# Performance work log

Hardware: AMD Instinct MI355X
Metric: run time of the kernel (lower is better)

Reference implementation:

```python
import jax, jax.numpy as jnp
import numpy as np

N, E, D = 40000, 640000, 128  # n_nodes, n_edges, hidden_dim
EPS = 1e-5  # equinox RMSNorm default eps


def setup_inputs() -> dict:
    key = jax.random.key(0)
    k1, k2, k3, k4 = jax.random.split(key, 4)
    x = jax.random.normal(k1, (N, D), dtype=jnp.float32)
    e = jax.random.randint(k2, (E, 2), 0, N)  # [E,2] int, col0=src, col1=dst
    W = jax.random.normal(k3, (D, D), dtype=jnp.float32) / np.sqrt(D).astype(np.float32)
    b = jax.random.normal(k4, (D,), dtype=jnp.float32) * 0.01
    g = jnp.ones((D,), dtype=jnp.float32)   # RMSNorm weight
    rb = jnp.zeros((D,), dtype=jnp.float32)  # RMSNorm bias
    return {"x": x, "e": e, "W": W, "b": b, "g": g, "rb": rb}


def reference(x, e, W, b, g, rb):
    src, dst = e[:, 0], e[:, 1]
    # gather source nodes, per-edge linear + relu  -> [E, D]
    m = jax.nn.relu(x[src] @ W.T + b)
    n = x.shape[0]
    # degree (any column of segment_sum(ones_like(m)) is the scalar degree)
    deg = jax.ops.segment_sum(jnp.ones((e.shape[0],), x.dtype), dst, num_segments=n)
    # max-aggregate messages to destination nodes  -> [N, D]
    agg = jax.ops.segment_max(m, dst, num_segments=n)
    agg = jnp.where(deg[:, None] == 0, jnp.zeros((), x.dtype), agg)
    # residual + RMSNorm
    h = x + agg
    inv = jax.lax.rsqrt(jnp.mean(h * h, axis=-1, keepdims=True) + EPS)
    return h * inv * g + rb
```

## Files before the change

### kernel.cpp

```cpp
#include <hip/hip_runtime.h>
#include <hip/hip_bf16.h>

#define D 128
#define EPS 1e-5f

typedef __bf16 bf16x8 __attribute__((ext_vector_type(8)));
typedef __bf16 bf16x4 __attribute__((ext_vector_type(4)));
typedef float  f32x4  __attribute__((ext_vector_type(4)));

__global__ __launch_bounds__(256) void prep_kernel(
    const float* __restrict__ W, __bf16* __restrict__ Wb,
    int* __restrict__ counts, int n)
{
    const int tid = blockIdx.x * 256 + threadIdx.x;

    if (tid < 4096) {
        float4 v = ((const float4*)W)[tid];
        bf16x4 h;
        h[0] = (__bf16)v.x; h[1] = (__bf16)v.y;
        h[2] = (__bf16)v.z; h[3] = (__bf16)v.w;
        ((bf16x4*)Wb)[tid] = h;
    }
    for (int i = tid; i < n; i += 4096)
        counts[i] = 0;
}

__global__ __launch_bounds__(256) void gemm_kernel(
    const float* __restrict__ x, const __bf16* __restrict__ Wb,
    const float* __restrict__ b, __bf16* __restrict__ y,
    const int* __restrict__ e, int* __restrict__ counts,
    int n, int E)
{
    __shared__ __attribute__((aligned(16))) float xs[64][132];

    const int tid  = threadIdx.x;
    const int row0b = blockIdx.x * 64;

    for (int i = tid; i < 2048; i += 256) {
        int r = i >> 5, q = i & 31;
        int gr = row0b + r;
        float4 v = make_float4(0.f, 0.f, 0.f, 0.f);
        if (gr < n) v = ((const float4*)x)[(size_t)gr * 32 + q];
        *(float4*)&xs[r][q * 4] = v;
    }

    {
        const int base   = blockIdx.x * 256 + tid;
        const int stride = gridDim.x * 256;
        for (int i = base; i < E; i += stride)
            atomicAdd(&counts[e[2 * i + 1]], 1);
    }
    __syncthreads();

    const int w  = tid >> 6;
    const int l  = tid & 63;
    const int lr = l & 15;
    const int lk = l >> 4;
    const int row0 = row0b + w * 16;

    bf16x8 a[4];
#pragma unroll
    for (int ks = 0; ks < 4; ks++) {
        const float* p = &xs[w * 16 + lr][ks * 32 + lk * 8];
        float4 v0 = *(const float4*)p;
        float4 v1 = *(const float4*)(p + 4);
        bf16x8 t;
        t[0] = (__bf16)v0.x; t[1] = (__bf16)v0.y;
        t[2] = (__bf16)v0.z; t[3] = (__bf16)v0.w;
        t[4] = (__bf16)v1.x; t[5] = (__bf16)v1.y;
        t[6] = (__bf16)v1.z; t[7] = (__bf16)v1.w;
        a[ks] = t;
    }

#pragma unroll
    for (int ct = 0; ct < 8; ct++) {
        f32x4 acc = {0.f, 0.f, 0.f, 0.f};
#pragma unroll
        for (int ks = 0; ks < 4; ks++) {
            bf16x8 bf = *(const bf16x8*)(Wb + (ct * 16 + lr) * D + ks * 32 + lk * 8);
            acc = __builtin_amdgcn_mfma_f32_16x16x32_bf16(a[ks], bf, acc, 0, 0, 0);
        }
        const int col  = ct * 16 + lr;
        const float bias = b[col];
        const int gr0  = row0 + lk * 4;
#pragma unroll
        for (int reg = 0; reg < 4; reg++) {
            int gr = gr0 + reg;
            if (gr < n)
                y[(size_t)gr * D + col] = (__bf16)fmaxf(acc[reg] + bias, 0.f);
        }
    }
}

__global__ __launch_bounds__(256) void scan_partial_kernel(
    const int* __restrict__ counts, int* __restrict__ row_start,
    int* __restrict__ partials, int n)
{
    __shared__ int s[256];
    const int tid = threadIdx.x;
    const int i = blockIdx.x * 256 + tid;
    int v = (i < n) ? counts[i] : 0;
    s[tid] = v;
    __syncthreads();
    for (int off = 1; off < 256; off <<= 1) {
        int add = (tid >= off) ? s[tid - off] : 0;
        __syncthreads();
        s[tid] += add;
        __syncthreads();
    }
    if (i < n) row_start[i] = s[tid] - v;
    if (tid == 255) partials[blockIdx.x] = s[255];
}

__global__ __launch_bounds__(256) void scan_add_kernel(
    int* __restrict__ row_start, const int* __restrict__ partials,
    int* __restrict__ cursor, int n, int nb)
{
    __shared__ int s[256];
    const int tid = threadIdx.x;
    int v = (tid < nb) ? partials[tid] : 0;
    s[tid] = v;
    __syncthreads();
    for (int off = 1; off < 256; off <<= 1) {
        int add = (tid >= off) ? s[tid - off] : 0;
        __syncthreads();
        s[tid] += add;
        __syncthreads();
    }
    int off0 = (blockIdx.x == 0) ? 0 : s[blockIdx.x - 1];

    if (blockIdx.x == 0 && tid == 0)
        row_start[n] = s[255];

    int i = blockIdx.x * 256 + tid;
    if (i < n) {
        int val = row_start[i] + off0;
        row_start[i] = val;
        cursor[i]    = val;
    }
}

__global__ __launch_bounds__(256) void place_kernel(
    const int* __restrict__ e, int* __restrict__ cursor,
    unsigned short* __restrict__ sorted_src, int E)
{
    int i = blockIdx.x * 256 + threadIdx.x;
    if (i < E) {
        int2 ed = ((const int2*)e)[i];
        int pos = atomicAdd(&cursor[ed.y], 1);
        sorted_src[pos] = (unsigned short)ed.x;
    }
}

__global__ __launch_bounds__(256) void seg_max_finalize_kernel(
    const int* __restrict__ row_start, const unsigned short* __restrict__ ssrc,
    const unsigned int* __restrict__ ybu, const float* __restrict__ x,
    const float* __restrict__ g, const float* __restrict__ rb,
    float* __restrict__ out, int n)
{
    int row  = blockIdx.x * 4 + (threadIdx.x >> 6);
    int lane = threadIdx.x & 63;
    if (row >= n) return;

    const int start = row_start[row];
    const int end   = row_start[row + 1];

    float mx = 0.f, my = 0.f;
    int k = start;
    const int end8 = start + ((end - start) & ~7);
    for (; k < end8; k += 8) {
        unsigned int u0, u1, u2, u3, u4, u5, u6, u7;
        {
            int s0 = ssrc[k + 0], s1 = ssrc[k + 1], s2 = ssrc[k + 2], s3 = ssrc[k + 3];
            int s4 = ssrc[k + 4], s5 = ssrc[k + 5], s6 = ssrc[k + 6], s7 = ssrc[k + 7];
            u0 = ybu[(size_t)s0 * 64 + lane];
            u1 = ybu[(size_t)s1 * 64 + lane];
            u2 = ybu[(size_t)s2 * 64 + lane];
            u3 = ybu[(size_t)s3 * 64 + lane];
            u4 = ybu[(size_t)s4 * 64 + lane];
            u5 = ybu[(size_t)s5 * 64 + lane];
            u6 = ybu[(size_t)s6 * 64 + lane];
            u7 = ybu[(size_t)s7 * 64 + lane];
        }
        mx = fmaxf(mx, fmaxf(fmaxf(__uint_as_float(u0 << 16), __uint_as_float(u1 << 16)),
                             fmaxf(__uint_as_float(u2 << 16), __uint_as_float(u3 << 16))));
        mx = fmaxf(mx, fmaxf(fmaxf(__uint_as_float(u4 << 16), __uint_as_float(u5 << 16)),
                             fmaxf(__uint_as_float(u6 << 16), __uint_as_float(u7 << 16))));
        my = fmaxf(my, fmaxf(fmaxf(__uint_as_float(u0 & 0xffff0000u), __uint_as_float(u1 & 0xffff0000u)),
                             fmaxf(__uint_as_float(u2 & 0xffff0000u), __uint_as_float(u3 & 0xffff0000u))));
        my = fmaxf(my, fmaxf(fmaxf(__uint_as_float(u4 & 0xffff0000u), __uint_as_float(u5 & 0xffff0000u)),
                             fmaxf(__uint_as_float(u6 & 0xffff0000u), __uint_as_float(u7 & 0xffff0000u))));
    }
    for (; k < end; k++) {
        int s0 = ssrc[k];
        unsigned int u0 = ybu[(size_t)s0 * 64 + lane];
        mx = fmaxf(mx, __uint_as_float(u0 << 16));
        my = fmaxf(my, __uint_as_float(u0 & 0xffff0000u));
    }

    float2 xv = ((const float2*)(x + (size_t)row * D))[lane];
    float hx = xv.x + mx;
    float hy = xv.y + my;

    float ss = hx * hx + hy * hy;
#pragma unroll
    for (int off = 1; off < 64; off <<= 1) ss += __shfl_xor(ss, off);

    float inv = rsqrtf(ss * (1.0f / (float)D) + EPS);

    float2 gv = ((const float2*)g)[lane];
    float2 rv = ((const float2*)rb)[lane];
    float2 o  = make_float2(hx * inv * gv.x + rv.x,
                            hy * inv * gv.y + rv.y);
    ((float2*)(out + (size_t)row * D))[lane] = o;
}

extern "C" void kernel_launch(void* const* d_in, const int* in_sizes, int n_in,
                              void* d_out, int out_size, void* d_ws, size_t ws_size,
                              hipStream_t stream)
{
    const float* x  = (const float*)d_in[0];
    const int*   e  = (const int*)  d_in[1];
    const float* W  = (const float*)d_in[2];
    const float* b  = (const float*)d_in[3];
    const float* g  = (const float*)d_in[4];
    const float* rb = (const float*)d_in[5];
    float* out = (float*)d_out;

    const int n = in_sizes[0] / D;
    const int E = in_sizes[1] / 2;

    char* ws = (char*)d_ws;
    __bf16* y        = (__bf16*)(ws);
    int*   counts    = (int*)  (ws + 10240000);
    int*   row_start = (int*)  (ws + 10400000);
    int*   cursor    = (int*)  (ws + 10560256);
    unsigned short* sorted_src = (unsigned short*)(ws + 10720256);
    int*   partials  = (int*)  (ws + 12000256);
    __bf16* Wb       = (__bf16*)(ws + 12001536);

    const int nb = (n + 255) / 256;

    prep_kernel<<<16, 256, 0, stream>>>(W, Wb, counts, n);

    gemm_kernel<<<(n + 63) / 64, 256, 0, stream>>>(x, Wb, b, y, e, counts, n, E);

    scan_partial_kernel<<<nb, 256, 0, stream>>>(counts, row_start, partials, n);
    scan_add_kernel<<<nb, 256, 0, stream>>>(row_start, partials, cursor, n, nb);
    place_kernel<<<(E + 255) / 256, 256, 0, stream>>>(e, cursor, sorted_src, E);

    seg_max_finalize_kernel<<<(n + 3) / 4, 256, 0, stream>>>(
        row_start, sorted_src, (const unsigned int*)y, x, g, rb, out, n);
}
```

Measured before the change: 189.0 us.

## Split degree histogram out of GEMM and retile GEMM to register-resident operands

Moves the edge-degree atomic histogram out of the GEMM kernel into its own kernel. The GEMM now loads x rows directly into registers with no shared-memory staging or barrier. Each block covers 32 rows, and each wave computes a 16x64 tile with its W fragments preloaded into registers. This removes the LDS round trip and the barrier stall behind the atomics, at the cost of an extra launch and more register pressure. The segment-max loop change is cosmetic.

```diff
diff --git a/kernel.cpp b/kernel.cpp
--- a/kernel.cpp
+++ b/kernel.cpp
@@ -25,69 +25,77 @@
         counts[i] = 0;
 }
 
-__global__ __launch_bounds__(256) void gemm_kernel(
+__global__ __launch_bounds__(256) void hist_kernel(
+    const int* __restrict__ e, int* __restrict__ counts, int E)
+{
+    int i = blockIdx.x * 256 + threadIdx.x;
+    if (i < E) {
+        int2 ed = ((const int2*)e)[i];
+        atomicAdd(&counts[ed.y], 1);
+    }
+}
+
+__global__ __launch_bounds__(256, 2) void gemm_kernel(
     const float* __restrict__ x, const __bf16* __restrict__ Wb,
-    const float* __restrict__ b, __bf16* __restrict__ y,
-    const int* __restrict__ e, int* __restrict__ counts,
-    int n, int E)
-{
-    __shared__ __attribute__((aligned(16))) float xs[64][132];
-
+    const float* __restrict__ b, __bf16* __restrict__ y, int n)
+{
     const int tid  = threadIdx.x;
-    const int row0b = blockIdx.x * 64;
-
-    for (int i = tid; i < 2048; i += 256) {
-        int r = i >> 5, q = i & 31;
-        int gr = row0b + r;
-        float4 v = make_float4(0.f, 0.f, 0.f, 0.f);
-        if (gr < n) v = ((const float4*)x)[(size_t)gr * 32 + q];
-        *(float4*)&xs[r][q * 4] = v;
-    }
-
-    {
-        const int base   = blockIdx.x * 256 + tid;
-        const int stride = gridDim.x * 256;
-        for (int i = base; i < E; i += stride)
-            atomicAdd(&counts[e[2 * i + 1]], 1);
-    }
-    __syncthreads();
-
-    const int w  = tid >> 6;
-    const int l  = tid & 63;
-    const int lr = l & 15;
-    const int lk = l >> 4;
-    const int row0 = row0b + w * 16;
+    const int w    = tid >> 6;
+    const int l    = tid & 63;
+    const int lr   = l & 15;
+    const int lk   = l >> 4;
+    const int row0 = blockIdx.x * 32 + (w & 1) * 16;
+    const int col0 = (w >> 1) * 64;
+
+    int ar = row0 + lr;
+    if (ar >= n) ar = n - 1;
+    const float* xr = x + (size_t)ar * D;
+
+    float4 xv[8];
+#pragma unroll
+    for (int ks = 0; ks < 4; ks++) {
+        xv[2 * ks]     = *(const float4*)(xr + ks * 32 + lk * 8);
+        xv[2 * ks + 1] = *(const float4*)(xr + ks * 32 + lk * 8 + 4);
+    }
+    bf16x8 wf[4][4];
+#pragma unroll
+    for (int ct = 0; ct < 4; ct++)
+#pragma unroll
+        for (int ks = 0; ks < 4; ks++)
+            wf[ct][ks] = *(const bf16x8*)
+                (Wb + (size_t)(col0 + ct * 16 + lr) * D + ks * 32 + lk * 8);
 
     bf16x8 a[4];
 #pragma unroll
     for (int ks = 0; ks < 4; ks++) {
-        const float* p = &xs[w * 16 + lr][ks * 32 + lk * 8];
-        float4 v0 = *(const float4*)p;
-        float4 v1 = *(const float4*)(p + 4);
         bf16x8 t;
-        t[0] = (__bf16)v0.x; t[1] = (__bf16)v0.y;
-        t[2] = (__bf16)v0.z; t[3] = (__bf16)v0.w;
-        t[4] = (__bf16)v1.x; t[5] = (__bf16)v1.y;
-        t[6] = (__bf16)v1.z; t[7] = (__bf16)v1.w;
+        t[0] = (__bf16)xv[2 * ks].x;     t[1] = (__bf16)xv[2 * ks].y;
+        t[2] = (__bf16)xv[2 * ks].z;     t[3] = (__bf16)xv[2 * ks].w;
+        t[4] = (__bf16)xv[2 * ks + 1].x; t[5] = (__bf16)xv[2 * ks + 1].y;
+        t[6] = (__bf16)xv[2 * ks + 1].z; t[7] = (__bf16)xv[2 * ks + 1].w;
         a[ks] = t;
     }
 
-#pragma unroll
-    for (int ct = 0; ct < 8; ct++) {
-        f32x4 acc = {0.f, 0.f, 0.f, 0.f};
-#pragma unroll
-        for (int ks = 0; ks < 4; ks++) {
-            bf16x8 bf = *(const bf16x8*)(Wb + (ct * 16 + lr) * D + ks * 32 + lk * 8);
-            acc = __builtin_amdgcn_mfma_f32_16x16x32_bf16(a[ks], bf, acc, 0, 0, 0);
-        }
-        const int col  = ct * 16 + lr;
+    f32x4 acc[4];
+#pragma unroll
+    for (int ct = 0; ct < 4; ct++) acc[ct] = (f32x4){0.f, 0.f, 0.f, 0.f};
+#pragma unroll
+    for (int ks = 0; ks < 4; ks++)
+#pragma unroll
+        for (int ct = 0; ct < 4; ct++)
+            acc[ct] = __builtin_amdgcn_mfma_f32_16x16x32_bf16(
+                a[ks], wf[ct][ks], acc[ct], 0, 0, 0);
+
+#pragma unroll
+    for (int ct = 0; ct < 4; ct++) {
+        const int col  = col0 + ct * 16 + lr;
         const float bias = b[col];
         const int gr0  = row0 + lk * 4;
 #pragma unroll
         for (int reg = 0; reg < 4; reg++) {
             int gr = gr0 + reg;
             if (gr < n)
-                y[(size_t)gr * D + col] = (__bf16)fmaxf(acc[reg] + bias, 0.f);
+                y[(size_t)gr * D + col] = (__bf16)fmaxf(acc[ct][reg] + bias, 0.f);
         }
     }
 }
@@ -169,19 +177,16 @@
     int k = start;
     const int end8 = start + ((end - start) & ~7);
     for (; k < end8; k += 8) {
-        unsigned int u0, u1, u2, u3, u4, u5, u6, u7;
-        {
-            int s0 = ssrc[k + 0], s1 = ssrc[k + 1], s2 = ssrc[k + 2], s3 = ssrc[k + 3];
-            int s4 = ssrc[k + 4], s5 = ssrc[k + 5], s6 = ssrc[k + 6], s7 = ssrc[k + 7];
-            u0 = ybu[(size_t)s0 * 64 + lane];
-            u1 = ybu[(size_t)s1 * 64 + lane];
-            u2 = ybu[(size_t)s2 * 64 + lane];
-            u3 = ybu[(size_t)s3 * 64 + lane];
-            u4 = ybu[(size_t)s4 * 64 + lane];
-            u5 = ybu[(size_t)s5 * 64 + lane];
-            u6 = ybu[(size_t)s6 * 64 + lane];
-            u7 = ybu[(size_t)s7 * 64 + lane];
-        }
+        int s0 = ssrc[k + 0], s1 = ssrc[k + 1], s2 = ssrc[k + 2], s3 = ssrc[k + 3];
+        int s4 = ssrc[k + 4], s5 = ssrc[k + 5], s6 = ssrc[k + 6], s7 = ssrc[k + 7];
+        unsigned int u0 = ybu[(size_t)s0 * 64 + lane];
+        unsigned int u1 = ybu[(size_t)s1 * 64 + lane];
+        unsigned int u2 = ybu[(size_t)s2 * 64 + lane];
+        unsigned int u3 = ybu[(size_t)s3 * 64 + lane];
+        unsigned int u4 = ybu[(size_t)s4 * 64 + lane];
+        unsigned int u5 = ybu[(size_t)s5 * 64 + lane];
+        unsigned int u6 = ybu[(size_t)s6 * 64 + lane];
+        unsigned int u7 = ybu[(size_t)s7 * 64 + lane];
         mx = fmaxf(mx, fmaxf(fmaxf(__uint_as_float(u0 << 16), __uint_as_float(u1 << 16)),
                              fmaxf(__uint_as_float(u2 << 16), __uint_as_float(u3 << 16))));
         mx = fmaxf(mx, fmaxf(fmaxf(__uint_as_float(u4 << 16), __uint_as_float(u5 << 16)),
@@ -243,7 +248,9 @@
 
     prep_kernel<<<16, 256, 0, stream>>>(W, Wb, counts, n);
 
-    gemm_kernel<<<(n + 63) / 64, 256, 0, stream>>>(x, Wb, b, y, e, counts, n, E);
+    hist_kernel<<<(E + 255) / 256, 256, 0, stream>>>(e, counts, E);
+
+    gemm_kernel<<<(n + 31) / 32, 256, 0, stream>>>(x, Wb, b, y, n);
 
     scan_partial_kernel<<<nb, 256, 0, stream>>>(counts, row_start, partials, n);
     scan_add_kernel<<<nb, 256, 0, stream>>>(row_start, partials, cursor, n, nb);
```

Result: no change. 191.0 us (+1.1%).
